# Performance work log

Measured on AMD Instinct MI355X. Metric: run time of the kernel, lower is better.

The kernel has to match this reference:

```python
import jax, jax.numpy as jnp
import numpy as np

N = 50000        # num_nodes
E = 800000       # num_edges
D = 128          # hidden_dim == attention_dim
H = 4            # heads
DK = D // H      # d_k per head
STEP = 0.25      # args.step_size
NSTEPS = 4       # euler steps for t: 0 -> 1


def setup_inputs() -> dict:
    key = jax.random.key(0)
    k0, k1, k2, k3 = jax.random.split(key, 4)
    x = jax.random.normal(k0, (N, D), dtype=jnp.float32)
    edge_index = jax.random.randint(k1, (2, E), 0, N, dtype=jnp.int64)
    W_Q = jax.random.normal(k2, (D, D), dtype=jnp.float32) * 0.02
    b_Q = jnp.zeros((D,), jnp.float32)
    W_K = jax.random.normal(k3, (D, D), dtype=jnp.float32) * 0.02
    b_K = jnp.zeros((D,), jnp.float32)
    return {"x": x, "W_Q": W_Q, "b_Q": b_Q, "W_K": W_K, "b_K": b_K,
            "edge_index": edge_index}


def _segment_softmax(scores, seg, num_segments):
    # numerically-stable softmax over edges grouped by seg (dst node)
    m = jax.ops.segment_max(scores, seg, num_segments=num_segments)
    e = jnp.exp(scores - m[seg])
    s = jax.ops.segment_sum(e, seg, num_segments=num_segments)
    return e / (s[seg] + 1e-16)


def reference(x, W_Q, b_Q, W_K, b_K, edge_index):
    src, dst = edge_index[0], edge_index[1]
    # multi-head Q/K projections: [N, H, DK]
    q = (x @ W_Q + b_Q).reshape(N, H, DK)
    k = (x @ W_K + b_K).reshape(N, H, DK)
    # per-edge scaled-dot scores: [E, H]
    scores = jnp.sum(q[src] * k[dst], axis=-1) / np.sqrt(DK).astype(np.float32)
    # edge softmax normalized over edge[attention_norm_idx]=edge[1] (dst)
    att = _segment_softmax(scores, dst, N)          # [E, H]
    att_mean = jnp.mean(att, axis=1)                # [E] head-averaged, as in GRAND odefunc

    # fixed-step Euler integration of dx/dt = A x - x with A = attention spmm
    def euler_step(state, _):
        ax = jax.ops.segment_sum(att_mean[:, None] * state[dst], src,
                                 num_segments=N)    # ax[src] += att * x[dst]
        return state + STEP * (ax - state), None

    z, _ = jax.lax.scan(euler_step, x, None, length=NSTEPS)
    return z
```

## Files before the change

### kernel.cpp

```cpp
#include <hip/hip_runtime.h>
#include <hip/hip_fp16.h>

#define NODES 50000
#define EDGES 800000
#define HID   128
#define HEADS 4
#define SCORE_SCALE 0.17677669529663687f

#define NBUCK ((NODES + 255) >> 8)
#define CHUNK 4096

typedef unsigned int       u32;
typedef unsigned short     u16;
typedef unsigned long long u64;

typedef __attribute__((ext_vector_type(8))) short bf16x8;
typedef __attribute__((ext_vector_type(4))) float f32x4;

__device__ __forceinline__ u16 f2bf(float f) {
    u32 u = __builtin_bit_cast(u32, f);
    return (u16)((u + 0x7FFFu + ((u >> 16) & 1u)) >> 16);
}
__device__ __forceinline__ float bflo(u32 u) { return __builtin_bit_cast(float, u << 16); }
__device__ __forceinline__ float bfhi(u32 u) { return __builtin_bit_cast(float, u & 0xFFFF0000u); }
__device__ __forceinline__ float bdot2(u32 a, u32 b) {
    return bflo(a) * bflo(b) + bfhi(a) * bfhi(b);
}
__device__ __forceinline__ float2 h2f2(u32 u) {
    __half2 h = __builtin_bit_cast(__half2, u);
    return __half22float2(h);
}
__device__ __forceinline__ u32 f2h2(float a, float b) {
    __half2 h = __floats2half2_rn(a, b);
    return __builtin_bit_cast(u32, h);
}

__global__ __launch_bounds__(256) void wprep(
    const float* __restrict__ Wq, const float* __restrict__ Wk,
    u16* __restrict__ Wqt, u16* __restrict__ Wkt)
{
    int e   = blockIdx.x * 256 + threadIdx.x;
    int mat = e >> 14;
    int idx = e & 16383;
    int k  = idx >> 7;
    int nn = idx & 127;
    const float* W = mat ? Wk : Wq;
    u16*        Wt = mat ? Wkt : Wqt;
    Wt[nn * 128 + k] = f2bf(W[idx]);
}

__global__ __launch_bounds__(256) void gemm_qk_mfma(
    const float* __restrict__ x,
    const u16* __restrict__ Wqt, const float* __restrict__ bq,
    const u16* __restrict__ Wkt, const float* __restrict__ bk,
    u16* __restrict__ qb, u16* __restrict__ kb, u16* __restrict__ xh, int n)
{
    const int l  = threadIdx.x & 63;
    const int w  = threadIdx.x >> 6;
    const int lr = l & 15;
    const int kg = l >> 4;

    const int arow   = blockIdx.x * 64 + w * 16 + lr;
    const bool av    = (arow < n);
    const int  arowc = av ? arow : (n - 1);

    bf16x8 afrag[4];
    #pragma unroll
    for (int ks = 0; ks < 4; ++ks) {
        const float* px = x + (size_t)arowc * HID + ks * 32 + kg * 8;
        float4 p0 = *(const float4*)px;
        float4 p1 = *(const float4*)(px + 4);
        uint4 pk;
        pk.x = (u32)f2bf(p0.x) | ((u32)f2bf(p0.y) << 16);
        pk.y = (u32)f2bf(p0.z) | ((u32)f2bf(p0.w) << 16);
        pk.z = (u32)f2bf(p1.x) | ((u32)f2bf(p1.y) << 16);
        pk.w = (u32)f2bf(p1.z) | ((u32)f2bf(p1.w) << 16);
        afrag[ks] = __builtin_bit_cast(bf16x8, pk);
        if (av) {
            uint4 ph;
            ph.x = f2h2(p0.x, p0.y);
            ph.y = f2h2(p0.z, p0.w);
            ph.z = f2h2(p1.x, p1.y);
            ph.w = f2h2(p1.z, p1.w);
            *(uint4*)(xh + (size_t)arow * HID + ks * 32 + kg * 8) = ph;
        }
    }

    #pragma unroll
    for (int mat = 0; mat < 2; ++mat) {
        const u16*   Wt   = mat ? Wkt : Wqt;
        const float* bias = mat ? bk : bq;
        u16*         outp = mat ? kb : qb;

        #pragma unroll
        for (int cb = 0; cb < 8; ++cb) {
            float bc = bias[cb * 16 + lr];
            f32x4 acc = {bc, bc, bc, bc};
            #pragma unroll
            for (int ks = 0; ks < 4; ++ks) {
                bf16x8 bfrag = __builtin_bit_cast(bf16x8,
                    *(const uint4*)(Wt + (size_t)(cb * 16 + lr) * 128 + ks * 32 + kg * 8));
                acc = __builtin_amdgcn_mfma_f32_16x16x32_bf16(afrag[ks], bfrag, acc, 0, 0, 0);
            }
            #pragma unroll
            for (int reg = 0; reg < 4; ++reg) {
                int gr = blockIdx.x * 64 + w * 16 + kg * 4 + reg;
                if (gr < n) outp[(size_t)gr * HID + cb * 16 + lr] = f2bf(acc[reg]);
            }
        }
    }
}

__global__ __launch_bounds__(256) void hist_kernel(
    const int* __restrict__ ei, int* __restrict__ deg)
{
    int i = blockIdx.x * 256 + threadIdx.x;
    if (i < EDGES) atomicAdd(&deg[ei[i]], 1);
}

__global__ __launch_bounds__(1024) void scan1(
    const int* __restrict__ deg, int* __restrict__ off,
    int* __restrict__ part, int n)
{
    __shared__ int sd[1024];
    int t = threadIdx.x, i = blockIdx.x * 1024 + t;
    int v = (i < n) ? deg[i] : 0;
    sd[t] = v;
    __syncthreads();
    #pragma unroll
    for (int o = 1; o < 1024; o <<= 1) {
        int a = (t >= o) ? sd[t - o] : 0;
        __syncthreads();
        sd[t] += a;
        __syncthreads();
    }
    if (i < n) off[i] = sd[t] - v;
    if (t == 1023) part[blockIdx.x] = sd[1023];
}

__global__ __launch_bounds__(64) void scan2(int* __restrict__ part,
                                            int* __restrict__ off_n, int nb)
{
    int t = threadIdx.x;
    int v = (t < nb) ? part[t] : 0;
    int orig = v;
    #pragma unroll
    for (int o = 1; o < 64; o <<= 1) {
        int a = __shfl_up(v, o);
        if (t >= o) v += a;
    }
    if (t < nb) part[t] = v - orig;
    if (t == 63) *off_n = v;
}

__global__ __launch_bounds__(1024) void scan3(
    int* __restrict__ off, int* __restrict__ bcur,
    const int* __restrict__ part, int n)
{
    int i = blockIdx.x * 1024 + threadIdx.x;
    if (i < n) {
        int o = off[i] + part[blockIdx.x];
        off[i] = o;
        if ((i & 255) == 0) bcur[i >> 8] = o;
    }
}

__global__ __launch_bounds__(256) void bin_edges(
    const int* __restrict__ ei, int* __restrict__ bcur, u32* __restrict__ tmp)
{
    __shared__ u32 buf[CHUNK];
    __shared__ int hist[NBUCK];
    __shared__ int lcur[NBUCK];

    const int t  = threadIdx.x;
    const int e0 = blockIdx.x * CHUNK;
    const int e1 = (e0 + CHUNK < EDGES) ? e0 + CHUNK : EDGES;
    const int cnt = e1 - e0;

    for (int b = t; b < NBUCK; b += 256) hist[b] = 0;
    __syncthreads();

    for (int i = t; i < cnt; i += 256) {
        int src = ei[e0 + i];
        int dst = ei[EDGES + e0 + i];
        buf[i] = (u32)dst | ((u32)(src & 255) << 16) | ((u32)(src >> 8) << 24);
        atomicAdd(&hist[src >> 8], 1);
    }
    __syncthreads();

    for (int b = t; b < NBUCK; b += 256) {
        int h = hist[b];
        lcur[b] = h ? atomicAdd(&bcur[b], h) : 0;
    }
    __syncthreads();

    for (int i = t; i < cnt; i += 256) {
        u32 pk  = buf[i];
        int b   = pk >> 24;
        int pos = atomicAdd(&lcur[b], 1);
        tmp[pos] = pk & 0x00FFFFFFu;
    }
}

__global__ __launch_bounds__(256) void place_edges(
    const u32* __restrict__ tmp, const int* __restrict__ off,
    u32* __restrict__ epack, int n)
{
    __shared__ int lcur[256];
    const int t     = threadIdx.x;
    const int nbase = blockIdx.x << 8;
    const int nend  = (nbase + 256 < n) ? nbase + 256 : n;

    if (nbase + t < nend) lcur[t] = off[nbase + t];
    __syncthreads();

    const int s0 = off[nbase];
    const int s1 = off[nend];
    for (int i = s0 + t; i < s1; i += 256) {
        u32 pk    = tmp[i];
        int local = pk >> 16;
        int pos   = atomicAdd(&lcur[local], 1);
        epack[pos] = pk & 0xFFFFu;
    }
}

__global__ __launch_bounds__(256) void score_csr(
    const u16* __restrict__ qb, const u16* __restrict__ kb,
    const int* __restrict__ off, const u32* __restrict__ ccol,
    u16* __restrict__ evals16, float* __restrict__ nsum, int n)
{
    const int wv   = (blockIdx.x * 256 + threadIdx.x) >> 6;
    const int lane = threadIdx.x & 63;
    const int l16  = lane & 15;
    const int grp  = lane >> 4;
    if (wv >= n) return;

    const int beg = off[wv];
    const int end = off[wv + 1];

    uint4 qv = *(const uint4*)(qb + (size_t)wv * HID + l16 * 8);

    for (int j = beg; j < end; j += 16) {
        u32 d[4]; uint4 kv[4];
        #pragma unroll
        for (int u = 0; u < 4; ++u) {
            int e  = j + grp + u * 4;
            int ec = (e < end) ? e : (end - 1);
            d[u] = ccol[ec];
        }
        #pragma unroll
        for (int u = 0; u < 4; ++u)
            kv[u] = *(const uint4*)(kb + (size_t)d[u] * HID + l16 * 8);
        #pragma unroll
        for (int u = 0; u < 4; ++u) {
            int e = j + grp + u * 4;
            float p = bdot2(qv.x, kv[u].x) + bdot2(qv.y, kv[u].y) +
                      bdot2(qv.z, kv[u].z) + bdot2(qv.w, kv[u].w);
            p += __shfl_xor(p, 1);
            p += __shfl_xor(p, 2);
            if (e < end && (l16 & 3) == 0) {
                int head = l16 >> 2;
                float ev = __expf(p * SCORE_SCALE);
                evals16[(size_t)e * HEADS + head] = f2bf(ev);
                atomicAdd(&nsum[(size_t)d[u] * HEADS + head], ev);
            }
        }
    }
}

__global__ __launch_bounds__(256) void finalize_kernel(
    const u16* __restrict__ evals16, const float* __restrict__ nsum,
    u32* __restrict__ epack)
{
    int pos = blockIdx.x * 256 + threadIdx.x;
    if (pos >= EDGES) return;
    u32 dst = epack[pos];
    u64 ev8 = *(const u64*)(evals16 + (size_t)pos * HEADS);
    u32 lo = (u32)ev8, hi = (u32)(ev8 >> 32);
    float4 sv = *(const float4*)(nsum + (size_t)dst * HEADS);
    float am = 0.25f * (bflo(lo) / (sv.x + 1e-16f) + bfhi(lo) / (sv.y + 1e-16f) +
                        bflo(hi) / (sv.z + 1e-16f) + bfhi(hi) / (sv.w + 1e-16f));
    epack[pos] = dst | ((u32)f2bf(am) << 16);
}

template<int FINAL>
__global__ __launch_bounds__(256) void spmv_h(
    const u16* __restrict__ inh, u16* __restrict__ outh,
    float* __restrict__ outf,
    const int* __restrict__ off, const u32* __restrict__ epack, int n)
{
    const int w    = (blockIdx.x * 256 + threadIdx.x) >> 6;
    const int lane = threadIdx.x & 63;
    if (w >= n) return;

    const int beg = off[w];
    const int end = off[w + 1];

    float ax = 0.f, ay = 0.f;
    for (int j = beg; j < end; j += 64) {
        int cnt = end - j; if (cnt > 64) cnt = 64;
        u32 e = 0;
        if (lane < cnt) e = epack[j + lane];

        int jj = 0;
        for (; jj + 8 <= cnt; jj += 8) {
            u32 ee[8], s[8];
            #pragma unroll
            for (int u = 0; u < 8; ++u) ee[u] = __shfl(e, jj + u);
            #pragma unroll
            for (int u = 0; u < 8; ++u)
                s[u] = *(const u32*)(inh + (size_t)(ee[u] & 0xFFFFu) * HID + lane * 2);
            #pragma unroll
            for (int u = 0; u < 8; ++u) {
                float vv = bfhi(ee[u]);
                float2 sv = h2f2(s[u]);
                ax += vv * sv.x;
                ay += vv * sv.y;
            }
        }
        for (; jj + 4 <= cnt; jj += 4) {
            u32 ee[4], s[4];
            #pragma unroll
            for (int u = 0; u < 4; ++u) ee[u] = __shfl(e, jj + u);
            #pragma unroll
            for (int u = 0; u < 4; ++u)
                s[u] = *(const u32*)(inh + (size_t)(ee[u] & 0xFFFFu) * HID + lane * 2);
            #pragma unroll
            for (int u = 0; u < 4; ++u) {
                float vv = bfhi(ee[u]);
                float2 sv = h2f2(s[u]);
                ax += vv * sv.x;
                ay += vv * sv.y;
            }
        }
        for (; jj < cnt; ++jj) {
            u32 ee = __shfl(e, jj);
            u32 s  = *(const u32*)(inh + (size_t)(ee & 0xFFFFu) * HID + lane * 2);
            float vv = bfhi(ee);
            float2 sv = h2f2(s);
            ax += vv * sv.x;
            ay += vv * sv.y;
        }
    }

    u32 zi = *(const u32*)(inh + (size_t)w * HID + lane * 2);
    float2 xi = h2f2(zi);
    const float ox = 0.75f * xi.x + 0.25f * ax;
    const float oy = 0.75f * xi.y + 0.25f * ay;
    if (FINAL) {
        float2 o; o.x = ox; o.y = oy;
        *(float2*)(outf + (size_t)w * HID + lane * 2) = o;
    } else {
        *(u32*)(outh + (size_t)w * HID + lane * 2) = f2h2(ox, oy);
    }
}

extern "C" void kernel_launch(void* const* d_in, const int* in_sizes, int n_in,
                              void* d_out, int out_size, void* d_ws, size_t ws_size,
                              hipStream_t stream)
{
    (void)in_sizes; (void)n_in; (void)out_size; (void)ws_size;

    const float* x  = (const float*)d_in[0];
    const float* Wq = (const float*)d_in[1];
    const float* bq = (const float*)d_in[2];
    const float* Wk = (const float*)d_in[3];
    const float* bk = (const float*)d_in[4];
    const int*   ei = (const int*)d_in[5];
    float* out = (float*)d_out;

    const int N = NODES, E = EDGES;
    const size_t ROWB_B = (size_t)N * HID * 2;

    char* ws = (char*)d_ws;
    u16*   qb    = (u16*)(ws);
    u16*   kb    = (u16*)(ws + ROWB_B);
    u16*   z1    = (u16*)(ws);
    u16*   z2    = (u16*)(ws + ROWB_B);
    ws += 2 * ROWB_B;
    u16*   xh    = (u16*)ws;  ws += ROWB_B;
    u16*   evals16 = (u16*)ws;
    u16*   z3    = (u16*)ws;  ws += (size_t)E * HEADS * 4;
    float* nsum  = (float*)ws; ws += (size_t)N * HEADS * 4;
    int*   deg   = (int*)ws;   ws += (size_t)N * 4;
    int*   off   = (int*)ws;   ws += ((size_t)(N + 1) * 4 + 255) & ~255ull;
    int*   bcur  = (int*)ws;   ws += ((size_t)NBUCK * 4 + 255) & ~255ull;
    int*   part  = (int*)ws;   ws += 256;
    u32*   epack = (u32*)ws;   ws += (size_t)E * 4;
    u32*   tmp   = (u32*)ws;   ws += (size_t)E * 4;
    u16*   Wqt   = (u16*)ws;   ws += (size_t)128 * 128 * 2;
    u16*   Wkt   = (u16*)ws;   ws += (size_t)128 * 128 * 2;

    hipMemsetAsync(nsum, 0, (size_t)N * HEADS * 4 + (size_t)N * 4, stream);

    wprep<<<128, 256, 0, stream>>>(Wq, Wk, Wqt, Wkt);

    gemm_qk_mfma<<<(N + 63) / 64, 256, 0, stream>>>(
        x, Wqt, bq, Wkt, bk, qb, kb, xh, N);

    hist_kernel<<<E / 256, 256, 0, stream>>>(ei, deg);

    const int nb = (N + 1023) / 1024;
    scan1<<<nb, 1024, 0, stream>>>(deg, off, part, N);
    scan2<<<1, 64, 0, stream>>>(part, off + N, nb);
    scan3<<<nb, 1024, 0, stream>>>(off, bcur, part, N);

    bin_edges<<<(E + CHUNK - 1) / CHUNK, 256, 0, stream>>>(ei, bcur, tmp);
    place_edges<<<NBUCK, 256, 0, stream>>>(tmp, off, epack, N);

    score_csr<<<(N * 64 + 255) / 256, 256, 0, stream>>>(
        qb, kb, off, epack, evals16, nsum, N);

    finalize_kernel<<<E / 256, 256, 0, stream>>>(evals16, nsum, epack);

    const int sg = (N * 64 + 255) / 256;
    spmv_h<0><<<sg, 256, 0, stream>>>(xh, z1, nullptr, off, epack, N);
    spmv_h<0><<<sg, 256, 0, stream>>>(z1, z2, nullptr, off, epack, N);
    spmv_h<0><<<sg, 256, 0, stream>>>(z2, z3, nullptr, off, epack, N);
    spmv_h<1><<<sg, 256, 0, stream>>>(z3, nullptr, out, off, epack, N);
}
```

Measured before the change: 290.2 us.

## Slice feature matrix into column blocks so SpMV gathers stay cache-resident

Stores the half-precision node features as four column slices of 32 values each, laid out slice-major, and rewrites the SpMV so each 16-lane group handles one node for one slice. Each kernel block covers 16 nodes within a single slice, so the gathered working set per slice is a quarter of the full matrix and is more likely to stay in L2/MALL. Edge-list loads and output stores switch to nontemporal hints. The cost is that the edge list is read four times, once per slice, and each gather is only 64 bytes.

New measurement: 352.5 us. 21.5% more time.

```diff
diff --git a/kernel.cpp b/kernel.cpp
--- a/kernel.cpp
+++ b/kernel.cpp
@@ -9,6 +9,8 @@
 
 #define NBUCK ((NODES + 255) >> 8)
 #define CHUNK 4096
+
+#define NSLICE 4
 
 typedef unsigned int       u32;
 typedef unsigned short     u16;
@@ -82,7 +84,7 @@
             ph.y = f2h2(p0.z, p0.w);
             ph.z = f2h2(p1.x, p1.y);
             ph.w = f2h2(p1.z, p1.w);
-            *(uint4*)(xh + (size_t)arow * HID + ks * 32 + kg * 8) = ph;
+            *(uint4*)(xh + ((size_t)ks * n + arow) * 32 + kg * 8) = ph;
         }
     }
 
@@ -284,32 +286,36 @@
 }
 
 template<int FINAL>
-__global__ __launch_bounds__(256) void spmv_h(
+__global__ __launch_bounds__(256) void spmv_x(
     const u16* __restrict__ inh, u16* __restrict__ outh,
     float* __restrict__ outf,
     const int* __restrict__ off, const u32* __restrict__ epack, int n)
 {
-    const int w    = (blockIdx.x * 256 + threadIdx.x) >> 6;
-    const int lane = threadIdx.x & 63;
-    if (w >= n) return;
+    const int tid   = threadIdx.x;
+    const int l16   = tid & 15;
+    const int grpb  = tid & 48;
+    const int slice = blockIdx.x & 3;
+    const int w     = (blockIdx.x >> 2) * 16 + (tid >> 4);
+
+    const u32* inq = (const u32*)(inh + (size_t)slice * n * 32);
 
     const int beg = off[w];
     const int end = off[w + 1];
 
     float ax = 0.f, ay = 0.f;
-    for (int j = beg; j < end; j += 64) {
-        int cnt = end - j; if (cnt > 64) cnt = 64;
+    for (int j = beg; j < end; j += 16) {
+        int cnt = end - j; if (cnt > 16) cnt = 16;
         u32 e = 0;
-        if (lane < cnt) e = epack[j + lane];
+        if (l16 < cnt) e = __builtin_nontemporal_load(epack + j + l16);
 
         int jj = 0;
         for (; jj + 8 <= cnt; jj += 8) {
             u32 ee[8], s[8];
             #pragma unroll
-            for (int u = 0; u < 8; ++u) ee[u] = __shfl(e, jj + u);
+            for (int u = 0; u < 8; ++u) ee[u] = __shfl(e, grpb + jj + u);
             #pragma unroll
             for (int u = 0; u < 8; ++u)
-                s[u] = *(const u32*)(inh + (size_t)(ee[u] & 0xFFFFu) * HID + lane * 2);
+                s[u] = inq[(size_t)(ee[u] & 0xFFFFu) * 16 + l16];
             #pragma unroll
             for (int u = 0; u < 8; ++u) {
                 float vv = bfhi(ee[u]);
@@ -321,10 +327,10 @@
         for (; jj + 4 <= cnt; jj += 4) {
             u32 ee[4], s[4];
             #pragma unroll
-            for (int u = 0; u < 4; ++u) ee[u] = __shfl(e, jj + u);
+            for (int u = 0; u < 4; ++u) ee[u] = __shfl(e, grpb + jj + u);
             #pragma unroll
             for (int u = 0; u < 4; ++u)
-                s[u] = *(const u32*)(inh + (size_t)(ee[u] & 0xFFFFu) * HID + lane * 2);
+                s[u] = inq[(size_t)(ee[u] & 0xFFFFu) * 16 + l16];
             #pragma unroll
             for (int u = 0; u < 4; ++u) {
                 float vv = bfhi(ee[u]);
@@ -334,8 +340,8 @@
             }
         }
         for (; jj < cnt; ++jj) {
-            u32 ee = __shfl(e, jj);
-            u32 s  = *(const u32*)(inh + (size_t)(ee & 0xFFFFu) * HID + lane * 2);
+            u32 ee = __shfl(e, grpb + jj);
+            u32 s  = inq[(size_t)(ee & 0xFFFFu) * 16 + l16];
             float vv = bfhi(ee);
             float2 sv = h2f2(s);
             ax += vv * sv.x;
@@ -343,15 +349,18 @@
         }
     }
 
-    u32 zi = *(const u32*)(inh + (size_t)w * HID + lane * 2);
+    u32 zi = inq[(size_t)w * 16 + l16];
     float2 xi = h2f2(zi);
     const float ox = 0.75f * xi.x + 0.25f * ax;
     const float oy = 0.75f * xi.y + 0.25f * ay;
+
     if (FINAL) {
         float2 o; o.x = ox; o.y = oy;
-        *(float2*)(outf + (size_t)w * HID + lane * 2) = o;
+        __builtin_nontemporal_store(__builtin_bit_cast(u64, o),
+            (u64*)(outf + (size_t)w * HID + slice * 32 + l16 * 2));
     } else {
-        *(u32*)(outh + (size_t)w * HID + lane * 2) = f2h2(ox, oy);
+        __builtin_nontemporal_store(f2h2(ox, oy),
+            (u32*)outh + ((size_t)slice * n + w) * 16 + l16);
     }
 }
 
@@ -413,9 +422,9 @@
 
     finalize_kernel<<<E / 256, 256, 0, stream>>>(evals16, nsum, epack);
 
-    const int sg = (N * 64 + 255) / 256;
-    spmv_h<0><<<sg, 256, 0, stream>>>(xh, z1, nullptr, off, epack, N);
-    spmv_h<0><<<sg, 256, 0, stream>>>(z1, z2, nullptr, off, epack, N);
-    spmv_h<0><<<sg, 256, 0, stream>>>(z2, z3, nullptr, off, epack, N);
-    spmv_h<1><<<sg, 256, 0, stream>>>(z3, nullptr, out, off, epack, N);
-}
+    const int sgrid = NSLICE * ((N + 15) / 16);
+    spmv_x<0><<<sgrid, 256, 0, stream>>>(xh, z1, nullptr, off, epack, N);
+    spmv_x<0><<<sgrid, 256, 0, stream>>>(z1, z2, nullptr, off, epack, N);
+    spmv_x<0><<<sgrid, 256, 0, stream>>>(z2, z3, nullptr, off, epack, N);
+    spmv_x<1><<<sgrid, 256, 0, stream>>>(z3, nullptr, out, off, epack, N);
+}
```
